# Performance work log

Hardware: AMD Instinct MI355X
Metric: run time of the kernel (lower is better)

## Reference

```python
import jax, jax.numpy as jnp
import numpy as np
from math import sqrt

NUM_HEADS = 16
DIM_MODEL = 1024


def setup_inputs() -> dict:
    key = jax.random.key(0)
    ks = jax.random.split(key, 12)
    B, S, D, M = 4, 1024, DIM_MODEL, 64
    bound = 1.0 / sqrt(D)
    def lin_w(k):
        return jax.random.uniform(k, (D, D), jnp.float32, -bound, bound)
    def lin_b(k):
        return jax.random.uniform(k, (D,), jnp.float32, -bound, bound)
    return {
        "query": jax.random.normal(ks[0], (B, S, D), jnp.float32),
        "key": jax.random.normal(ks[1], (B, S, D), jnp.float32),
        "value": jax.random.normal(ks[2], (B, S, D), jnp.float32),
        "mask": jax.random.randint(ks[3], (1, B, S, M), 0, 2).astype(jnp.float32),
        "Wq": lin_w(ks[4]), "bq": lin_b(ks[5]),
        "Wk": lin_w(ks[6]), "bk": lin_b(ks[7]),
        "Wv": lin_w(ks[8]), "bv": lin_b(ks[9]),
        "Wo": lin_w(ks[10]),
    }


def reference(query, key, value, mask, Wq, bq, Wk, bk, Wv, bv, Wo):
    B, S, D = query.shape
    H = NUM_HEADS
    d = D // H
    # projections + head split, permute(2,0,1,3) -> [H,B,S,d]
    q = (query @ Wq.T + bq).reshape(B, S, H, d).transpose(2, 0, 1, 3)
    k = (key @ Wk.T + bk).reshape(B, S, H, d).transpose(2, 0, 1, 3)
    v = (value @ Wv.T + bv).reshape(B, S, H, d).transpose(2, 0, 1, 3)
    attn = jnp.einsum("hbqd,hbkd->hbqk", q, k) / sqrt(d)  # [H,B,S,S]
    # custom mask: mask.repeat(H,1,1,1) then mask @ mask^T / sqrt(m).
    # Identical per-head, so compute once on [B,S,m] and broadcast over H.
    m2d = mask[0]  # [B,S,m]
    mm = jnp.einsum("bqm,bkm->bqk", m2d, m2d) / sqrt(m2d.shape[-1])
    attn = jnp.where(mm[None] == 0, jnp.float32(-1e9), attn)
    w = jax.nn.softmax(attn, axis=-1)  # dropout is identity in eval mode
    x = jnp.einsum("hbqk,hbkd->hbqd", w, v)  # [H,B,S,d]
    # torch: permute(1,2,0,3) -> [B,S,H,d]; transpose(1,2) -> [B,H,S,d];
    # contiguous().view(B,-1,H*d) -- row-major reshape (mixes head/seq layout, replicated faithfully)
    x = jnp.transpose(x, (1, 0, 2, 3))  # [B,H,S,d]
    x = x.reshape(B, -1, H * d)
    return x @ Wo.T
```

## Files before the change

kernel.cpp:

```cpp
#include <hip/hip_runtime.h>

typedef unsigned int u32;
typedef unsigned short u16;
typedef unsigned long long u64;
typedef __attribute__((ext_vector_type(8))) short s16x8;
typedef __attribute__((ext_vector_type(8))) __bf16 bf16x8;
typedef __attribute__((ext_vector_type(4))) float f32x4;
typedef __attribute__((ext_vector_type(16))) float f32x16;
typedef __attribute__((ext_vector_type(4))) u32 u32x4;

#define WSMB (1ull << 20)
#define QSC 0.18033688011112042f

static __device__ __forceinline__ u16 f2bf(float f) {
  u32 u = __builtin_bit_cast(u32, f);
  return (u16)((u + 0x7fffu + ((u >> 16) & 1u)) >> 16);
}

static __device__ __forceinline__ u32 pkbf(float lo, float hi) {
  u32 r;
  asm("v_cvt_pk_bf16_f32 %0, %1, %2" : "=v"(r) : "v"(lo), "v"(hi));
  return r;
}

static __device__ __forceinline__ float ex2(float x) {
  float r;
  asm("v_exp_f32 %0, %1" : "=v"(r) : "v"(x));
  return r;
}

static __device__ __forceinline__ f32x4 mfma16x16(s16x8 a, s16x8 b, f32x4 c) {
  return __builtin_amdgcn_mfma_f32_16x16x32_bf16(
      __builtin_bit_cast(bf16x8, a), __builtin_bit_cast(bf16x8, b), c, 0, 0, 0);
}

static __device__ __forceinline__ f32x16 mfma32x32(s16x8 a, s16x8 b, f32x16 c) {
  return __builtin_amdgcn_mfma_f32_32x32x16_bf16(
      __builtin_bit_cast(bf16x8, a), __builtin_bit_cast(bf16x8, b), c, 0, 0, 0);
}

#define GLOAD_LDS16(g, l)                                                      \
  __builtin_amdgcn_global_load_lds(                                            \
      (const __attribute__((address_space(1))) u32*)(const void*)(g),          \
      (__attribute__((address_space(3))) u32*)(void*)(l), 16, 0, 0)

__global__ __launch_bounds__(256) void k_prep(
    const float* __restrict__ xq, const float* __restrict__ xk,
    const float* __restrict__ xv, const float* __restrict__ wq,
    const float* __restrict__ wk, const float* __restrict__ wv,
    const float* __restrict__ wo, const float* __restrict__ mask,
    u16* __restrict__ oxq, u16* __restrict__ oxk, u16* __restrict__ oxv,
    u16* __restrict__ owq, u16* __restrict__ owk, u16* __restrict__ owv,
    u16* __restrict__ owo, u64* __restrict__ bits) {
  const int y = blockIdx.y;
  if (y >= 3 && blockIdx.x >= 1024) return;
  if (y == 7) {
    int w = threadIdx.x >> 6, l = threadIdx.x & 63;
    int r = blockIdx.x * 4 + w;
    float v = mask[(size_t)r * 64 + l];
    u64 bl = __ballot(v != 0.0f);
    if (l == 0) bits[r] = bl;
    return;
  }
  const float* s;
  u16* d;
  switch (y) {
    case 0: s = xq; d = oxq; break;
    case 1: s = xk; d = oxk; break;
    case 2: s = xv; d = oxv; break;
    case 3: s = wq; d = owq; break;
    case 4: s = wk; d = owk; break;
    case 5: s = wv; d = owv; break;
    default: s = wo; d = owo; break;
  }
  int i = (blockIdx.x * 256 + threadIdx.x) * 4;
  float4 v = *(const float4*)(s + i);
  u64 p = (u64)f2bf(v.x) | ((u64)f2bf(v.y) << 16) | ((u64)f2bf(v.z) << 32) |
          ((u64)f2bf(v.w) << 48);
  *(u64*)(d + i) = p;
}

__global__ __launch_bounds__(256) void k_mm(const u64* __restrict__ bits,
                                            u64* __restrict__ MB) {
  int wv = threadIdx.x >> 6, l = threadIdx.x & 63;
  int qg = blockIdx.x * 4 + wv;
  u64 bq = bits[qg];
  const u64* bb = bits + (qg & ~1023);
  u64* out = MB + (size_t)qg * 16;
  for (int kt = 0; kt < 16; kt++) {
    u64 bk = bb[kt * 64 + l];
    u64 m = __ballot((bq & bk) != 0ull);
    if (l == 0) out[kt] = m;
  }
}

static __device__ __forceinline__ void gemm_core(const u16* __restrict__ A,
                                                 const u16* __restrict__ Bw,
                                                 f32x4 (&acc)[4][4]) {
  __shared__ __attribute__((aligned(16))) u16 As[2][4096];
  __shared__ __attribute__((aligned(16))) u16 Bs[2][4096];
  const int t = threadIdx.x;
  const int l = t & 63, w = t >> 6, lr = l & 15, lk = l >> 4;
  const int amr = (w & 1) * 64, bnr = (w >> 1) * 64;
  const int c0 = t, c1 = t + 256;
  const int r0 = c0 >> 2, r1 = c1 >> 2;
  const int sw0 = ((c0 & 3) * 8) ^ ((r0 & 6) << 2);
  const int sw1 = ((c1 & 3) * 8) ^ ((r1 & 6) << 2);
  const u16* Ag0 = A + (size_t)r0 * 1024 + sw0;
  const u16* Ag1 = A + (size_t)r1 * 1024 + sw1;
  const u16* Bg0 = Bw + (size_t)r0 * 1024 + sw0;
  const u16* Bg1 = Bw + (size_t)r1 * 1024 + sw1;
  const int aswz = (lk * 16) ^ ((lr & 6) << 3);

  GLOAD_LDS16(Ag0, &As[0][c0 * 8]);
  GLOAD_LDS16(Ag1, &As[0][c1 * 8]);
  GLOAD_LDS16(Bg0, &Bs[0][c0 * 8]);
  GLOAD_LDS16(Bg1, &Bs[0][c1 * 8]);

  int cur = 0;
  for (int kt = 0; kt < 1024; kt += 32) {
    __syncthreads();
    if (kt < 992) {
      const int nxt = cur ^ 1;
      GLOAD_LDS16(Ag0 + kt + 32, &As[nxt][c0 * 8]);
      GLOAD_LDS16(Ag1 + kt + 32, &As[nxt][c1 * 8]);
      GLOAD_LDS16(Bg0 + kt + 32, &Bs[nxt][c0 * 8]);
      GLOAD_LDS16(Bg1 + kt + 32, &Bs[nxt][c1 * 8]);
    }
    const char* Ac = (const char*)As[cur];
    const char* Bc = (const char*)Bs[cur];
    s16x8 af[4], bf[4];
#pragma unroll
    for (int i = 0; i < 4; i++)
      af[i] = *(const s16x8*)(Ac + (amr + i * 16 + lr) * 64 + aswz);
#pragma unroll
    for (int j = 0; j < 4; j++)
      bf[j] = *(const s16x8*)(Bc + (bnr + j * 16 + lr) * 64 + aswz);
    __builtin_amdgcn_s_setprio(1);
#pragma unroll
    for (int i = 0; i < 4; i++)
#pragma unroll
      for (int j = 0; j < 4; j++)
        acc[i][j] = mfma16x16(af[i], bf[j], acc[i][j]);
    __builtin_amdgcn_s_setprio(0);
    cur ^= 1;
  }
}

__global__ __launch_bounds__(256) void k_qkv(
    const u16* __restrict__ Xq, const u16* __restrict__ Xk,
    const u16* __restrict__ Xv, const u16* __restrict__ Wqb,
    const u16* __restrict__ Wkb, const u16* __restrict__ Wvb,
    const float* __restrict__ bq, const float* __restrict__ bk,
    const float* __restrict__ bv, u16* __restrict__ Qo, u16* __restrict__ Ko,
    u16* __restrict__ V4) {
  const int bid0 = blockIdx.x;
  const int bid = (bid0 & 7) * 96 + (bid0 >> 3);
  const int proj = bid >> 8;
  const int rem = bid & 255;
  const int st = rem >> 3, dt = rem & 7;
  const u16* Xp = proj == 0 ? Xq : (proj == 1 ? Xk : Xv);
  const u16* Wp = proj == 0 ? Wqb : (proj == 1 ? Wkb : Wvb);
  const float* bias = proj == 0 ? bq : (proj == 1 ? bk : bv);
  const int t = threadIdx.x;
  const int l = t & 63, w = t >> 6, lr = l & 15, lk = l >> 4;
  const int amr = (w & 1) * 64, bnr = (w >> 1) * 64;
  f32x4 acc[4][4] = {};
  if (proj < 2) {
    const float sc = proj == 0 ? QSC : 1.0f;
    gemm_core(Wp + (size_t)dt * 131072, Xp + (size_t)st * 131072, acc);
    u16* O = proj ? Ko : Qo;
#pragma unroll
    for (int i = 0; i < 4; i++) {
      const int d0 = dt * 128 + amr + i * 16 + lk * 4;
      const int h = d0 >> 6, dd0 = d0 & 63;
      const float4 b4 = *(const float4*)(bias + d0);
#pragma unroll
      for (int j = 0; j < 4; j++) {
        const int s = st * 128 + bnr + j * 16 + lr;
        const int b_ = s >> 10, si = s & 1023;
        u32 e0 = pkbf((acc[i][j][0] + b4.x) * sc, (acc[i][j][1] + b4.y) * sc);
        u32 e1 = pkbf((acc[i][j][2] + b4.z) * sc, (acc[i][j][3] + b4.w) * sc);
        *(u64*)(O + ((size_t)((b_ * 16 + h) * 1024 + si)) * 64 + dd0) =
            (u64)e0 | ((u64)e1 << 32);
      }
    }
  } else {
    gemm_core(Xp + (size_t)st * 131072, Wp + (size_t)dt * 131072, acc);
#pragma unroll
    for (int i = 0; i < 4; i++) {
      const int s0 = st * 128 + amr + i * 16 + lk * 4;
      const int b_ = s0 >> 10, si = s0 & 1023;
      const int sblk = si >> 3, soff = si & 7;
#pragma unroll
      for (int j = 0; j < 4; j++) {
        const int d = dt * 128 + bnr + j * 16 + lr;
        const int h = d >> 6, dd = d & 63;
        const float bb = bias[d];
        u32 e0 = pkbf(acc[i][j][0] + bb, acc[i][j][1] + bb);
        u32 e1 = pkbf(acc[i][j][2] + bb, acc[i][j][3] + bb);
        *(u64*)(V4 + (size_t)(b_ * 16 + h) * 65536 +
                (size_t)(sblk * 64 + dd) * 8 + soff) =
            (u64)e0 | ((u64)e1 << 32);
      }
    }
  }
}

__global__ __launch_bounds__(256) void k_oproj(const u16* __restrict__ Xb,
                                               const u16* __restrict__ Wob,
                                               float* __restrict__ Out) {
  const int bid0 = blockIdx.x;
  const int bid = (bid0 & 7) * 32 + (bid0 >> 3);
  const int mb = bid >> 3, nb = bid & 7;
  f32x4 acc[4][4] = {};
  gemm_core(Xb + (size_t)mb * 131072, Wob + (size_t)nb * 131072, acc);
  const int t = threadIdx.x;
  const int l = t & 63, w = t >> 6, lr = l & 15, lk = l >> 4;
  const int amr = (w & 1) * 64, bnr = (w >> 1) * 64;
#pragma unroll
  for (int i = 0; i < 4; i++)
#pragma unroll
    for (int j = 0; j < 4; j++)
#pragma unroll
      for (int r = 0; r < 4; r++) {
        const int m = mb * 128 + amr + i * 16 + lk * 4 + r;
        const int n = nb * 128 + bnr + j * 16 + lr;
        Out[(size_t)m * 1024 + n] = acc[i][j][r];
      }
}

__global__ __launch_bounds__(256, 3) void k_attn(const u16* __restrict__ Qb,
                                                 const u16* __restrict__ Kb,
                                                 const u16* __restrict__ V4,
                                                 const u64* __restrict__ MB,
                                                 u16* __restrict__ xbuf) {
  __shared__ __attribute__((aligned(16))) float cmb[128 * 36];
  const int t = threadIdx.x, l = t & 63, w = t >> 6;
  const int q5 = l & 31, hi = l >> 5;
  const int wq = w & 1;
  const int kh = w >> 1;
  const int bid = (blockIdx.x & 7) * 128 + (blockIdx.x >> 3);
  const int qt = bid & 15, hb = bid >> 4;
  const int h = hb >> 2, b = hb & 3;
  const int s0 = qt * 64;
  const u16* Qhb = Qb + (size_t)(b * 16 + h) * 65536;
  const u16* Khb = Kb + (size_t)(b * 16 + h) * 65536;
  const u16* Vhb = V4 + (size_t)(b * 16 + h) * 65536;
  const int q = s0 + wq * 32 + q5;
  const u64* MBq = MB + ((size_t)b * 1024 + q) * 16;
  const int kt0 = kh * 8;

  s16x8 qf[4];
#pragma unroll
  for (int ds = 0; ds < 4; ds++)
    qf[ds] = *(const s16x8*)(Qhb + (size_t)q * 64 + ds * 16 + hi * 8);

  f32x16 xa0 = {}, xa1 = {};
  float ls = 0.f, m_ = -__builtin_inff();

  const u16* Kr0 = Khb + (size_t)q5 * 64 + hi * 8;
  const u16* Kr1 = Khb + (size_t)(32 + q5) * 64 + hi * 8;
  const u16* Vr0 = Vhb + (size_t)q5 * 8;
  const u16* Vr1 = Vhb + (size_t)(32 + q5) * 8;

  u64 mw = MBq[kt0];
  for (int i = 0; i < 8; i++) {
    const int kt = kt0 + i;
    const int ko = kt * 4096;
    const int vb = kt * 8 + hi;
    s16x8 k0[4], k1[4];
#pragma unroll
    for (int ds = 0; ds < 4; ds++) {
      k0[ds] = *(const s16x8*)(Kr0 + ko + ds * 16);
      k1[ds] = *(const s16x8*)(Kr1 + ko + ds * 16);
    }
    s16x8 v0[4], v1[4];
#pragma unroll
    for (int ks = 0; ks < 4; ks++) {
      v0[ks] = *(const s16x8*)(Vr0 + (size_t)(vb + 2 * ks) * 512);
      v1[ks] = *(const s16x8*)(Vr1 + (size_t)(vb + 2 * ks) * 512);
    }
    const u64 nw = MBq[kt0 + ((i + 1) & 7)];

    f32x16 z0 = {}, z1 = {};
    __builtin_amdgcn_s_setprio(1);
#pragma unroll
    for (int ds = 0; ds < 4; ds++) {
      z0 = mfma32x32(k0[ds], qf[ds], z0);
      z1 = mfma32x32(k1[ds], qf[ds], z1);
    }
    __builtin_amdgcn_s_setprio(0);

    float t0 = fmaxf(z0[0], z1[0]), t1 = fmaxf(z0[1], z1[1]);
    float t2 = fmaxf(z0[2], z1[2]), t3 = fmaxf(z0[3], z1[3]);
#pragma unroll
    for (int r = 4; r < 16; r += 4) {
      t0 = fmaxf(t0, fmaxf(z0[r], z1[r]));
      t1 = fmaxf(t1, fmaxf(z0[r + 1], z1[r + 1]));
      t2 = fmaxf(t2, fmaxf(z0[r + 2], z1[r + 2]));
      t3 = fmaxf(t3, fmaxf(z0[r + 3], z1[r + 3]));
    }
    float tm = fmaxf(fmaxf(t0, t1), fmaxf(t2, t3));
    tm = fmaxf(tm, __shfl_xor(tm, 32));
    if (tm > m_) {
      const float scl = ex2(m_ - tm);
      m_ = tm;
      ls *= scl;
      xa0 *= scl;
      xa1 *= scl;
    }

#pragma unroll
    for (int r = 0; r < 16; r++) z0[r] = ex2(z0[r] - m_);
#pragma unroll
    for (int r = 0; r < 16; r++) z1[r] = ex2(z1[r] - m_);
    if (!__all(mw == ~0ull)) {
      const u32 mh0 = (u32)(mw >> (hi * 4));
      const u32 mh1 = (u32)(mw >> (hi * 4 + 32));
#pragma unroll
      for (int r = 0; r < 16; r++) {
        const int bp = 8 * (r >> 2) + (r & 3);
        z0[r] = ((mh0 >> bp) & 1u) ? z0[r] : 0.f;
        z1[r] = ((mh1 >> bp) & 1u) ? z1[r] : 0.f;
      }
    }
    float ts = 0.f;
#pragma unroll
    for (int r = 0; r < 16; r++) ts += z0[r] + z1[r];
    ls += ts;

    u32 P0[2][4], P1[2][4];
#pragma unroll
    for (int qi = 0; qi < 4; qi++) {
      P0[0][qi] = pkbf(z0[4 * qi], z0[4 * qi + 1]);
      P1[0][qi] = pkbf(z0[4 * qi + 2], z0[4 * qi + 3]);
      P0[1][qi] = pkbf(z1[4 * qi], z1[4 * qi + 1]);
      P1[1][qi] = pkbf(z1[4 * qi + 2], z1[4 * qi + 3]);
    }

#pragma unroll
    for (int ks = 0; ks < 4; ks++) {
      const int kb_ = ks >> 1, qi0 = (ks & 1) * 2, qi1 = qi0 + 1;
      u32 w0 = P0[kb_][qi0], w2 = P0[kb_][qi1];
      u32 w1 = P1[kb_][qi0], w3 = P1[kb_][qi1];
      asm("v_permlane32_swap_b32 %0, %1" : "+v"(w0), "+v"(w2));
      asm("v_permlane32_swap_b32 %0, %1" : "+v"(w1), "+v"(w3));
      u32x4 fv;
      fv[0] = w0; fv[1] = w1; fv[2] = w2; fv[3] = w3;
      const s16x8 pb = __builtin_bit_cast(s16x8, fv);
      __builtin_amdgcn_s_setprio(1);
      xa0 = mfma32x32(v0[ks], pb, xa0);
      xa1 = mfma32x32(v1[ks], pb, xa1);
      __builtin_amdgcn_s_setprio(0);
    }
    mw = nw;
  }

  if (w >= 2) {
    float* p = &cmb[(size_t)((w - 2) * 64 + l) * 36];
    *(f32x16*)(p) = xa0;
    *(f32x16*)(p + 16) = xa1;
    p[32] = m_;
    p[33] = ls;
  }
  __syncthreads();
  if (w >= 2) return;
  {
    const float* p = &cmb[(size_t)(wq * 64 + l) * 36];
    const f32x16 xb0 = *(const f32x16*)(p);
    const f32x16 xb1 = *(const f32x16*)(p + 16);
    const float mb = p[32], lsb = p[33];
    const float m = fmaxf(m_, mb);
    const float sa = ex2(m_ - m), sb = ex2(mb - m);
    ls = ls * sa + lsb * sb;
    xa0 = xa0 * sa + xb0 * sb;
    xa1 = xa1 * sa + xb1 * sb;
  }

  ls += __shfl_xor(ls, 32);
  const float inv = 1.0f / ls;
  const size_t rowb = (size_t)b * 1048576 + (size_t)(h * 64 + (q >> 4)) * 1024 +
                      (size_t)(q & 15) * 64;
#pragma unroll
  for (int qi = 0; qi < 4; qi++) {
    u32 a0 = pkbf(xa0[4 * qi] * inv, xa0[4 * qi + 1] * inv);
    u32 a1 = pkbf(xa0[4 * qi + 2] * inv, xa0[4 * qi + 3] * inv);
    *(u64*)(xbuf + rowb + 8 * qi + 4 * hi) = (u64)a0 | ((u64)a1 << 32);
    u32 b0 = pkbf(xa1[4 * qi] * inv, xa1[4 * qi + 1] * inv);
    u32 b1 = pkbf(xa1[4 * qi + 2] * inv, xa1[4 * qi + 3] * inv);
    *(u64*)(xbuf + rowb + 32 + 8 * qi + 4 * hi) = (u64)b0 | ((u64)b1 << 32);
  }
}

extern "C" void kernel_launch(void* const* d_in, const int* in_sizes, int n_in,
                              void* d_out, int out_size, void* d_ws,
                              size_t ws_size, hipStream_t stream) {
  const float* query = (const float*)d_in[0];
  const float* key_ = (const float*)d_in[1];
  const float* value = (const float*)d_in[2];
  const float* mask = (const float*)d_in[3];
  const float* bq = (const float*)d_in[5];
  const float* bk = (const float*)d_in[7];
  const float* bv = (const float*)d_in[9];
  const float* Wq = (const float*)d_in[4];
  const float* Wk = (const float*)d_in[6];
  const float* Wv = (const float*)d_in[8];
  const float* Wo = (const float*)d_in[10];

  char* ws = (char*)d_ws;
  u16* Xq = (u16*)(ws + 0 * WSMB);
  u16* Xk = (u16*)(ws + 8 * WSMB);
  u16* Xv = (u16*)(ws + 16 * WSMB);
  u16* Wqb = (u16*)(ws + 24 * WSMB);
  u16* Wkb = (u16*)(ws + 26 * WSMB);
  u16* Wvb = (u16*)(ws + 28 * WSMB);
  u16* Wob = (u16*)(ws + 30 * WSMB);
  u16* Qb = (u16*)(ws + 32 * WSMB);
  u16* Kb = (u16*)(ws + 40 * WSMB);
  u16* V4 = (u16*)(ws + 48 * WSMB);
  u64* bits = (u64*)(ws + 56 * WSMB);
  u64* MBm = (u64*)(ws + 8 * WSMB);
  u16* xbuf = Xq;

  k_prep<<<dim3(4096, 8), 256, 0, stream>>>(query, key_, value, Wq, Wk, Wv, Wo,
                                            mask, Xq, Xk, Xv, Wqb, Wkb, Wvb,
                                            Wob, bits);
  k_qkv<<<768, 256, 0, stream>>>(Xq, Xk, Xv, Wqb, Wkb, Wvb, bq, bk, bv, Qb, Kb,
                                 V4);
  k_mm<<<1024, 256, 0, stream>>>(bits, MBm);
  k_attn<<<1024, 256, 0, stream>>>(Qb, Kb, V4, MBm, xbuf);
  k_oproj<<<256, 256, 0, stream>>>(xbuf, Wob, (float*)d_out);
}
```

Baseline: 130.5 us.

## Stage K/V tiles through swizzled LDS via direct global-to-LDS loads

The attention kernel now loads each K/V tile cooperatively into shared memory with global-to-LDS loads, using an XOR swizzle, instead of each wave reading K/V fragments directly from global memory. The fragments are then read from LDS right before each MFMA, and the combine buffer reuses the same shared allocation. Occupancy hint raised from 3 to 4 blocks per CU. This cuts register pressure and per-wave global traffic, but adds two block barriers per iteration and no double buffering, so load latency is exposed.

```diff
diff --git a/kernel.cpp b/kernel.cpp
--- a/kernel.cpp
+++ b/kernel.cpp
@@ -230,12 +230,12 @@
       }
 }
 
-__global__ __launch_bounds__(256, 3) void k_attn(const u16* __restrict__ Qb,
+__global__ __launch_bounds__(256, 4) void k_attn(const u16* __restrict__ Qb,
                                                  const u16* __restrict__ Kb,
                                                  const u16* __restrict__ V4,
                                                  const u64* __restrict__ MB,
                                                  u16* __restrict__ xbuf) {
-  __shared__ __attribute__((aligned(16))) float cmb[128 * 36];
+  __shared__ __attribute__((aligned(16))) u16 SMEM[16384];
   const int t = threadIdx.x, l = t & 63, w = t >> 6;
   const int q5 = l & 31, hi = l >> 5;
   const int wq = w & 1;
@@ -259,38 +259,47 @@
   f32x16 xa0 = {}, xa1 = {};
   float ls = 0.f, m_ = -__builtin_inff();
 
-  const u16* Kr0 = Khb + (size_t)q5 * 64 + hi * 8;
-  const u16* Kr1 = Khb + (size_t)(32 + q5) * 64 + hi * 8;
-  const u16* Vr0 = Vhb + (size_t)q5 * 8;
-  const u16* Vr1 = Vhb + (size_t)(32 + q5) * 8;
+  const int ca = t, cb_ = t + 256;
+  const int rA = ca >> 3, colA = (ca & 7) * 16;
+  const int rB = cb_ >> 3, colB = (cb_ & 7) * 16;
+  const int sA = colA ^ ((rA & 7) << 4);
+  const int sB = colB ^ ((rB & 7) << 4);
+  const u16* KgA = Khb + (size_t)rA * 64 + (sA >> 1);
+  const u16* KgB = Khb + (size_t)rB * 64 + (sB >> 1);
+  const u16* VgA = Vhb + (size_t)(sA >> 4) * 512 + rA * 8;
+  const u16* VgB = Vhb + (size_t)(sB >> 4) * 512 + rB * 8;
+
+  const int rbase = q5 * 128 + ((hi * 16) ^ ((q5 & 7) << 4));
+  const char* Kc = (const char*)(SMEM + kh * 4096);
+  const char* Vc = (const char*)(SMEM + 8192 + kh * 4096);
 
   u64 mw = MBq[kt0];
   for (int i = 0; i < 8; i++) {
-    const int kt = kt0 + i;
-    const int ko = kt * 4096;
-    const int vb = kt * 8 + hi;
-    s16x8 k0[4], k1[4];
+    if (i > 0) __syncthreads();
+    {
+      const int o0 = i * 4096, o1 = (8 + i) * 4096;
+      GLOAD_LDS16(KgA + o0, &SMEM[ca * 8]);
+      GLOAD_LDS16(KgB + o0, &SMEM[cb_ * 8]);
+      GLOAD_LDS16(KgA + o1, &SMEM[4096 + ca * 8]);
+      GLOAD_LDS16(KgB + o1, &SMEM[4096 + cb_ * 8]);
+      GLOAD_LDS16(VgA + o0, &SMEM[8192 + ca * 8]);
+      GLOAD_LDS16(VgB + o0, &SMEM[8192 + cb_ * 8]);
+      GLOAD_LDS16(VgA + o1, &SMEM[12288 + ca * 8]);
+      GLOAD_LDS16(VgB + o1, &SMEM[12288 + cb_ * 8]);
+    }
+    __syncthreads();
+    const u64 nw = MBq[kt0 + ((i + 1) & 7)];
+
+    f32x16 z0 = {}, z1 = {};
 #pragma unroll
     for (int ds = 0; ds < 4; ds++) {
-      k0[ds] = *(const s16x8*)(Kr0 + ko + ds * 16);
-      k1[ds] = *(const s16x8*)(Kr1 + ko + ds * 16);
-    }
-    s16x8 v0[4], v1[4];
-#pragma unroll
-    for (int ks = 0; ks < 4; ks++) {
-      v0[ks] = *(const s16x8*)(Vr0 + (size_t)(vb + 2 * ks) * 512);
-      v1[ks] = *(const s16x8*)(Vr1 + (size_t)(vb + 2 * ks) * 512);
-    }
-    const u64 nw = MBq[kt0 + ((i + 1) & 7)];
-
-    f32x16 z0 = {}, z1 = {};
-    __builtin_amdgcn_s_setprio(1);
-#pragma unroll
-    for (int ds = 0; ds < 4; ds++) {
-      z0 = mfma32x32(k0[ds], qf[ds], z0);
-      z1 = mfma32x32(k1[ds], qf[ds], z1);
-    }
-    __builtin_amdgcn_s_setprio(0);
+      s16x8 k0 = *(const s16x8*)(Kc + (rbase ^ (ds * 32)));
+      s16x8 k1 = *(const s16x8*)(Kc + 4096 + (rbase ^ (ds * 32)));
+      __builtin_amdgcn_s_setprio(1);
+      z0 = mfma32x32(k0, qf[ds], z0);
+      z1 = mfma32x32(k1, qf[ds], z1);
+      __builtin_amdgcn_s_setprio(0);
+    }
 
     float t0 = fmaxf(z0[0], z1[0]), t1 = fmaxf(z0[1], z1[1]);
     float t2 = fmaxf(z0[2], z1[2]), t3 = fmaxf(z0[3], z1[3]);
@@ -349,14 +358,18 @@
       u32x4 fv;
       fv[0] = w0; fv[1] = w1; fv[2] = w2; fv[3] = w3;
       const s16x8 pb = __builtin_bit_cast(s16x8, fv);
+      s16x8 v0 = *(const s16x8*)(Vc + (rbase ^ (ks * 32)));
+      s16x8 v1 = *(const s16x8*)(Vc + 4096 + (rbase ^ (ks * 32)));
       __builtin_amdgcn_s_setprio(1);
-      xa0 = mfma32x32(v0[ks], pb, xa0);
-      xa1 = mfma32x32(v1[ks], pb, xa1);
+      xa0 = mfma32x32(v0, pb, xa0);
+      xa1 = mfma32x32(v1, pb, xa1);
       __builtin_amdgcn_s_setprio(0);
     }
     mw = nw;
   }
 
+  float* cmb = (float*)SMEM;
+  __syncthreads();
   if (w >= 2) {
     float* p = &cmb[(size_t)((w - 2) * 64 + l) * 36];
     *(f32x16*)(p) = xa0;
```

After: 139.4 us. +6.9%, slower.
